# Performance work log

Hardware: AMD Instinct MI355X
Metric: run time of the kernel (lower is better)

Reference implementation:

```python
import jax, jax.numpy as jnp
import numpy as np

EMBED_DIM = 1024
NUM_HEADS = 16
HEAD_DIM = EMBED_DIM // NUM_HEADS
B, S = 2, 2048


def setup_inputs() -> dict:
    key = jax.random.key(0)
    ks = jax.random.split(key, 9)
    d = EMBED_DIM
    scale = 1.0 / np.sqrt(d)
    inp = {
        "x": jax.random.normal(ks[0], (B, S, d), dtype=jnp.float32),
        "mask": jnp.ones((B, S), dtype=jnp.int32),
        "Wq": jax.random.normal(ks[1], (d, d), dtype=jnp.float32) * scale,
        "bq": jnp.zeros((d,), dtype=jnp.float32),
        "Wk": jax.random.normal(ks[2], (d, d), dtype=jnp.float32) * scale,
        "bk": jnp.zeros((d,), dtype=jnp.float32),
        "Wv": jax.random.normal(ks[3], (d, d), dtype=jnp.float32) * scale,
        "bv": jnp.zeros((d,), dtype=jnp.float32),
        "Wo": jax.random.normal(ks[4], (d, d), dtype=jnp.float32) * scale,
        "bo": jnp.zeros((d,), dtype=jnp.float32),
    }
    return inp


def reference(x, mask, Wq, bq, Wk, bk, Wv, bv, Wo, bo):
    b, s, _ = x.shape
    # projections; torch Linear computes x @ W.T + b
    q = (x @ Wq.T + bq).reshape(b, s, NUM_HEADS, HEAD_DIM).transpose(0, 2, 1, 3)
    k = (x @ Wk.T + bk).reshape(b, s, NUM_HEADS, HEAD_DIM).transpose(0, 2, 1, 3)
    v = (x @ Wv.T + bv).reshape(b, s, NUM_HEADS, HEAD_DIM).transpose(0, 2, 1, 3)
    scores = jnp.einsum("bhqd,bhkd->bhqk", q, k) / np.sqrt(HEAD_DIM)  # (B,H,S,S)
    m = (mask == 0)[:, None, None, :]  # broadcast over heads and query pos
    scores = jnp.where(m, jnp.float32(-1e9), scores)
    attn = jax.nn.softmax(scores, axis=-1)
    out = jnp.einsum("bhqk,bhkd->bhqd", attn, v)
    out = out.transpose(0, 2, 1, 3).reshape(b, s, EMBED_DIM)
    return out @ Wo.T + bo
```

## Files before the change

### kernel.cpp

```cpp
#include <hip/hip_runtime.h>

#define EMBED 1024
#define NHEAD 16
#define HDIM  64
#define BB    2
#define SS    2048

typedef __bf16 bf16x8 __attribute__((ext_vector_type(8)));
typedef float  f32x4  __attribute__((ext_vector_type(4)));
typedef _Float16 f16x4 __attribute__((ext_vector_type(4)));
typedef __fp16 hf16x2 __attribute__((ext_vector_type(2)));

__device__ __forceinline__ unsigned short f2bf(float f) {
  union { float f; unsigned u; } v; v.f = f;
  unsigned r = v.u + 0x7fffu + ((v.u >> 16) & 1u);
  return (unsigned short)(r >> 16);
}

__device__ __forceinline__ unsigned short f2h(float f) {
  union { _Float16 h; unsigned short u; } t;
  t.h = (_Float16)f;
  return t.u;
}

__device__ __forceinline__ void g2l16(const unsigned short* g, unsigned short* l) {
  __builtin_amdgcn_global_load_lds(
      (const __attribute__((address_space(1))) unsigned int*)g,
      (__attribute__((address_space(3))) unsigned int*)l, 16, 0, 0);
}

__global__ __launch_bounds__(256)
void cvt5_kernel(const float* __restrict__ x,  const float* __restrict__ Wq,
                 const float* __restrict__ Wk, const float* __restrict__ Wv,
                 const float* __restrict__ Wo,
                 unsigned short* __restrict__ xb,  unsigned short* __restrict__ Wqb,
                 unsigned short* __restrict__ Wkb, unsigned short* __restrict__ Wvb,
                 unsigned short* __restrict__ Wob) {
  const int i = blockIdx.x * 256 + threadIdx.x;
  const float* src;
  unsigned short* dst;
  int j;
  if (i < (1 << 20)) {
    src = x; dst = xb; j = i;
  } else {
    const int t = i - (1 << 20);
    const int r = t >> 18;
    j = t & ((1 << 18) - 1);
    src = (r == 0) ? Wq : (r == 1) ? Wk : (r == 2) ? Wv : Wo;
    dst = (r == 0) ? Wqb : (r == 1) ? Wkb : (r == 2) ? Wvb : Wob;
  }
  const float4 f = ((const float4*)src)[j];
  ushort4 u;
  u.x = f2bf(f.x); u.y = f2bf(f.y); u.z = f2bf(f.z); u.w = f2bf(f.w);
  ((ushort4*)dst)[j] = u;
}

template <typename EpiFn>
__device__ __forceinline__
void gemm_core(const unsigned short* __restrict__ A,
               const unsigned short* __restrict__ Bm,
               int m0, int n0, EpiFn epi) {
  __shared__ unsigned short sA[128 * 64];
  __shared__ unsigned short sB[128 * 64];
  const int tid = threadIdx.x;
  const int l  = tid & 63;
  const int w  = tid >> 6;
  const int lm = l & 15;
  const int qd = l >> 4;
  const int wm = w & 1;
  const int wn = w >> 1;

  f32x4 acc[4][4];
#pragma unroll
  for (int i = 0; i < 4; ++i)
#pragma unroll
    for (int j = 0; j < 4; ++j) acc[i][j] = (f32x4){0.f, 0.f, 0.f, 0.f};

  for (int k0 = 0; k0 < EMBED; k0 += 64) {
#pragma unroll
    for (int i = 0; i < 4; ++i) {
      const int t = i * 256 + tid;
      const int r = t >> 3;
      const int c = (t & 7) ^ (r & 7);
      unsigned short* lp = &sA[(i * 256 + (w << 6)) * 8];
      g2l16(A + (m0 + r) * EMBED + k0 + c * 8, lp);
      unsigned short* lp2 = &sB[(i * 256 + (w << 6)) * 8];
      g2l16(Bm + (n0 + r) * EMBED + k0 + c * 8, lp2);
    }
    __syncthreads();
#pragma unroll
    for (int kk = 0; kk < 2; ++kk) {
      bf16x8 af[4], bfr[4];
#pragma unroll
      for (int mi = 0; mi < 4; ++mi) {
        const int R = wm * 64 + mi * 16 + lm;
        const int ch = R * 8 + (((kk << 2) + qd) ^ (R & 7));
        af[mi] = *(const bf16x8*)&sA[ch * 8];
      }
#pragma unroll
      for (int ni = 0; ni < 4; ++ni) {
        const int R = wn * 64 + ni * 16 + lm;
        const int ch = R * 8 + (((kk << 2) + qd) ^ (R & 7));
        bfr[ni] = *(const bf16x8*)&sB[ch * 8];
      }
#pragma unroll
      for (int mi = 0; mi < 4; ++mi)
#pragma unroll
        for (int ni = 0; ni < 4; ++ni)
          acc[mi][ni] = __builtin_amdgcn_mfma_f32_16x16x32_bf16(
              af[mi], bfr[ni], acc[mi][ni], 0, 0, 0);
    }
    __syncthreads();
  }

#pragma unroll
  for (int mi = 0; mi < 4; ++mi)
#pragma unroll
    for (int ni = 0; ni < 4; ++ni) {
      const int mb = m0 + wm * 64 + mi * 16 + qd * 4;
      const int n  = n0 + wn * 64 + ni * 16 + lm;
      epi(acc[mi][ni], mb, n);
    }
}

__global__ __launch_bounds__(256)
void gemm_qkv(const unsigned short* __restrict__ xb,
              const unsigned short* __restrict__ Wqb,
              const unsigned short* __restrict__ Wkb,
              const unsigned short* __restrict__ Wvb,
              const float* __restrict__ bq, const float* __restrict__ bk,
              const float* __restrict__ bv,
              unsigned short* __restrict__ Qb, unsigned short* __restrict__ Kb,
              unsigned short* __restrict__ VTb) {
  const int z = blockIdx.y;
  const int flat = blockIdx.x;
  if (z < 2) {
    const unsigned short* A = z ? Wkb : Wqb;
    const float* bias = z ? bk : bq;
    unsigned short* O = z ? Kb : Qb;
    const float scale = z ? 1.0f : 0.125f * 1.4426950408889634f;
    const int m0 = (flat >> 5) * 128;
    const int n0 = (flat & 31) * 128;
    gemm_core(A, xb, m0, n0, [&](const f32x4& v, int mb, int n) {
      const float4 bvv = *(const float4*)&bias[mb];
      const int h = mb >> 6, d0 = mb & 63;
      const int b = n >> 11, s = n & 2047;
      ushort4 u;
      u.x = f2bf((v.x + bvv.x) * scale); u.y = f2bf((v.y + bvv.y) * scale);
      u.z = f2bf((v.z + bvv.z) * scale); u.w = f2bf((v.w + bvv.w) * scale);
      *(ushort4*)&O[(((b * NHEAD + h) * SS) + s) * HDIM + d0] = u;
    });
  } else {
    const int m0 = (flat & 31) * 128;
    const int n0 = (flat >> 5) * 128;
    gemm_core(xb, Wvb, m0, n0, [&](const f32x4& v, int mb, int n) {
      const float bvv = bv[n];
      const int b = mb >> 11, s = mb & 2047;
      const int h = n >> 6, d = n & 63;
      ushort4 u;
      u.x = f2h(v.x + bvv); u.y = f2h(v.y + bvv);
      u.z = f2h(v.z + bvv); u.w = f2h(v.w + bvv);
      *(ushort4*)&VTb[(((b * NHEAD + h) * HDIM) + d) * SS + s] = u;
    });
  }
}

__global__ __launch_bounds__(256)
void gemm_out(const unsigned short* __restrict__ Wob,
              const unsigned short* __restrict__ Ob,
              const float* __restrict__ bo, float* __restrict__ out) {
  const int m0 = blockIdx.y * 128;
  const int n0 = blockIdx.x * 128;
  gemm_core(Wob, Ob, m0, n0, [&](const f32x4& v, int mb, int n) {
    const float4 bvv = *(const float4*)&bo[mb];
    float4 o;
    o.x = v.x + bvv.x; o.y = v.y + bvv.y; o.z = v.z + bvv.z; o.w = v.w + bvv.w;
    *(float4*)&out[n * EMBED + mb] = o;
  });
}

__global__ __launch_bounds__(256)
void attn_kernel(const unsigned short* __restrict__ Q,
                 const unsigned short* __restrict__ K,
                 const unsigned short* __restrict__ VT,
                 const int* __restrict__ mask,
                 unsigned short* __restrict__ Obuf) {
  __shared__ unsigned short sK[64 * 64];
  __shared__ unsigned short sV[64 * 64];
  const int tid = threadIdx.x;
  const int l = tid & 63, w = tid >> 6;
  const int lm = l & 15, qd = l >> 4;
  const int b = blockIdx.z, h = blockIdx.y;
  const int q0 = blockIdx.x * 64 + w * 16;
  const unsigned short* Qh = Q + ((b * NHEAD + h) * SS) * HDIM;
  const unsigned short* Kh = K + ((b * NHEAD + h) * SS) * HDIM;
  const unsigned short* Vh = VT + ((b * NHEAD + h) * HDIM) * SS;
  const int* mrow = mask + b * SS;

  const bf16x8 qf0 = *(const bf16x8*)&Qh[(q0 + lm) * HDIM + qd * 8];
  const bf16x8 qf1 = *(const bf16x8*)&Qh[(q0 + lm) * HDIM + 32 + qd * 8];

  f32x4 Od[4];
#pragma unroll
  for (int i = 0; i < 4; ++i) Od[i] = (f32x4){0.f, 0.f, 0.f, 0.f};
  float lsum = 0.f;

  for (int kb = 0; kb < SS; kb += 64) {
#pragma unroll
    for (int i = 0; i < 2; ++i) {
      const int t = i * 256 + tid;
      const int r = t >> 3;
      const int c = (t & 7) ^ (r & 7);
      g2l16(Kh + (kb + r) * HDIM + c * 8, &sK[(i * 256 + (w << 6)) * 8]);
      g2l16(Vh + r * SS + kb + c * 8, &sV[(i * 256 + (w << 6)) * 8]);
    }
    __syncthreads();

    int4 mk[4];
#pragma unroll
    for (int j = 0; j < 4; ++j) mk[j] = *(const int4*)&mrow[kb + j * 16 + qd * 4];

    f32x4 s[4];
#pragma unroll
    for (int j = 0; j < 4; ++j) {
      const int R = j * 16 + lm;
      const bf16x8 k0 = *(const bf16x8*)&sK[(R * 8 + (qd ^ (lm & 7))) * 8];
      const bf16x8 k1 = *(const bf16x8*)&sK[(R * 8 + ((4 + qd) ^ (lm & 7))) * 8];
      f32x4 t0 = (f32x4){0.f, 0.f, 0.f, 0.f};
      t0 = __builtin_amdgcn_mfma_f32_16x16x32_bf16(k0, qf0, t0, 0, 0, 0);
      t0 = __builtin_amdgcn_mfma_f32_16x16x32_bf16(k1, qf1, t0, 0, 0, 0);
      s[j] = t0;
    }

    f16x4 pf[4];
#pragma unroll
    for (int j = 0; j < 4; ++j) {
      const float p0 = mk[j].x ? exp2f(s[j][0]) : 0.f;
      const float p1 = mk[j].y ? exp2f(s[j][1]) : 0.f;
      const float p2 = mk[j].z ? exp2f(s[j][2]) : 0.f;
      const float p3 = mk[j].w ? exp2f(s[j][3]) : 0.f;
      lsum += (p0 + p1) + (p2 + p3);
      union { hf16x2 v[2]; f16x4 f; } pk;
      pk.v[0] = __builtin_amdgcn_cvt_pkrtz(p0, p1);
      pk.v[1] = __builtin_amdgcn_cvt_pkrtz(p2, p3);
      pf[j] = pk.f;
    }

#pragma unroll
    for (int dt = 0; dt < 4; ++dt) {
      const int row = dt * 16 + lm;
#pragma unroll
      for (int j = 0; j < 4; ++j) {
        const int ch = (j * 2 + (qd >> 1)) ^ (lm & 7);
        const f16x4 vf = *(const f16x4*)&sV[row * 64 + ch * 8 + (qd & 1) * 4];
        Od[dt] = __builtin_amdgcn_mfma_f32_16x16x16f16(vf, pf[j], Od[dt], 0, 0, 0);
      }
    }
    __syncthreads();
  }

  lsum += __shfl_xor(lsum, 16);
  lsum += __shfl_xor(lsum, 32);
  const float rinv = 1.f / lsum;
#pragma unroll
  for (int dt = 0; dt < 4; ++dt) {
    ushort4 u;
    u.x = f2bf(Od[dt][0] * rinv); u.y = f2bf(Od[dt][1] * rinv);
    u.z = f2bf(Od[dt][2] * rinv); u.w = f2bf(Od[dt][3] * rinv);
    *(ushort4*)&Obuf[(b * SS + q0 + lm) * EMBED + h * HDIM + dt * 16 + qd * 4] = u;
  }
}

extern "C" void kernel_launch(void* const* d_in, const int* in_sizes, int n_in,
                              void* d_out, int out_size, void* d_ws, size_t ws_size,
                              hipStream_t stream) {
  const float* x  = (const float*)d_in[0];
  const int* mask = (const int*)d_in[1];
  const float* Wq = (const float*)d_in[2];
  const float* bq = (const float*)d_in[3];
  const float* Wk = (const float*)d_in[4];
  const float* bk = (const float*)d_in[5];
  const float* Wv = (const float*)d_in[6];
  const float* bv = (const float*)d_in[7];
  const float* Wo = (const float*)d_in[8];
  const float* bo = (const float*)d_in[9];
  float* out = (float*)d_out;

  char* ws = (char*)d_ws;
  unsigned short* xb  = (unsigned short*)(ws);
  unsigned short* Wqb = (unsigned short*)(ws + 8u * 1024 * 1024);
  unsigned short* Wkb = Wqb + 1024 * 1024;
  unsigned short* Wvb = Wkb + 1024 * 1024;
  unsigned short* Wob = Wvb + 1024 * 1024;
  unsigned short* Qb  = (unsigned short*)(ws + 16u * 1024 * 1024);
  unsigned short* Kb  = Qb + 4u * 1024 * 1024;
  unsigned short* VTb = Kb + 4u * 1024 * 1024;
  unsigned short* Ob  = VTb + 4u * 1024 * 1024;

  cvt5_kernel<<<8192, 256, 0, stream>>>(x, Wq, Wk, Wv, Wo, xb, Wqb, Wkb, Wvb, Wob);
  gemm_qkv<<<dim3(256, 3), 256, 0, stream>>>(xb, Wqb, Wkb, Wvb, bq, bk, bv,
                                             Qb, Kb, VTb);
  attn_kernel<<<dim3(32, 16, 2), 256, 0, stream>>>(Qb, Kb, VTb, mask, Ob);
  gemm_out<<<dim3(32, 8), 256, 0, stream>>>(Wob, Ob, bo, out);
}
```

Measured before the change: 230.9 us.

## Double query rows per attention wave, precompute additive mask bias, swizzle GEMM tiles

Each attention wave now handles 32 query rows instead of 16, so every K/V tile loaded into LDS and every K fragment read feeds twice as many MFMAs. The int mask is turned once, in the conversion kernel, into an additive float bias that seeds the score accumulator, which removes the per-element select. exp2 now uses the hardware builtin. GEMM blocks are remapped in grouped tiles for better L2 reuse. The trade-offs are higher register pressure and only 512 attention blocks, which could lower occupancy.

```diff
diff --git a/kernel.cpp b/kernel.cpp
--- a/kernel.cpp
+++ b/kernel.cpp
@@ -11,6 +11,16 @@
 typedef _Float16 f16x4 __attribute__((ext_vector_type(4)));
 typedef __fp16 hf16x2 __attribute__((ext_vector_type(2)));
 
+#if defined(__has_builtin)
+#if __has_builtin(__builtin_amdgcn_exp2f)
+#define EXP2(x) __builtin_amdgcn_exp2f(x)
+#else
+#define EXP2(x) exp2f(x)
+#endif
+#else
+#define EXP2(x) exp2f(x)
+#endif
+
 __device__ __forceinline__ unsigned short f2bf(float f) {
   union { float f; unsigned u; } v; v.f = f;
   unsigned r = v.u + 0x7fffu + ((v.u >> 16) & 1u);
@@ -32,27 +42,36 @@
 __global__ __launch_bounds__(256)
 void cvt5_kernel(const float* __restrict__ x,  const float* __restrict__ Wq,
                  const float* __restrict__ Wk, const float* __restrict__ Wv,
-                 const float* __restrict__ Wo,
+                 const float* __restrict__ Wo, const int* __restrict__ mask,
                  unsigned short* __restrict__ xb,  unsigned short* __restrict__ Wqb,
                  unsigned short* __restrict__ Wkb, unsigned short* __restrict__ Wvb,
-                 unsigned short* __restrict__ Wob) {
+                 unsigned short* __restrict__ Wob, float* __restrict__ mbias) {
   const int i = blockIdx.x * 256 + threadIdx.x;
-  const float* src;
-  unsigned short* dst;
-  int j;
-  if (i < (1 << 20)) {
-    src = x; dst = xb; j = i;
+  if (i < (1 << 21)) {
+    const float* src;
+    unsigned short* dst;
+    int j;
+    if (i < (1 << 20)) {
+      src = x; dst = xb; j = i;
+    } else {
+      const int t = i - (1 << 20);
+      const int r = t >> 18;
+      j = t & ((1 << 18) - 1);
+      src = (r == 0) ? Wq : (r == 1) ? Wk : (r == 2) ? Wv : Wo;
+      dst = (r == 0) ? Wqb : (r == 1) ? Wkb : (r == 2) ? Wvb : Wob;
+    }
+    const float4 f = ((const float4*)src)[j];
+    ushort4 u;
+    u.x = f2bf(f.x); u.y = f2bf(f.y); u.z = f2bf(f.z); u.w = f2bf(f.w);
+    ((ushort4*)dst)[j] = u;
   } else {
-    const int t = i - (1 << 20);
-    const int r = t >> 18;
-    j = t & ((1 << 18) - 1);
-    src = (r == 0) ? Wq : (r == 1) ? Wk : (r == 2) ? Wv : Wo;
-    dst = (r == 0) ? Wqb : (r == 1) ? Wkb : (r == 2) ? Wvb : Wob;
-  }
-  const float4 f = ((const float4*)src)[j];
-  ushort4 u;
-  u.x = f2bf(f.x); u.y = f2bf(f.y); u.z = f2bf(f.z); u.w = f2bf(f.w);
-  ((ushort4*)dst)[j] = u;
+    const int j = i - (1 << 21);
+    const int4 m = ((const int4*)mask)[j];
+    float4 o;
+    o.x = m.x ? 0.f : -1e30f; o.y = m.y ? 0.f : -1e30f;
+    o.z = m.z ? 0.f : -1e30f; o.w = m.w ? 0.f : -1e30f;
+    ((float4*)mbias)[j] = o;
+  }
 }
 
 template <typename EpiFn>
@@ -82,10 +101,8 @@
       const int t = i * 256 + tid;
       const int r = t >> 3;
       const int c = (t & 7) ^ (r & 7);
-      unsigned short* lp = &sA[(i * 256 + (w << 6)) * 8];
-      g2l16(A + (m0 + r) * EMBED + k0 + c * 8, lp);
-      unsigned short* lp2 = &sB[(i * 256 + (w << 6)) * 8];
-      g2l16(Bm + (n0 + r) * EMBED + k0 + c * 8, lp2);
+      g2l16(A + (m0 + r) * EMBED + k0 + c * 8, &sA[(i * 256 + (w << 6)) * 8]);
+      g2l16(Bm + (n0 + r) * EMBED + k0 + c * 8, &sB[(i * 256 + (w << 6)) * 8]);
     }
     __syncthreads();
 #pragma unroll
@@ -121,6 +138,13 @@
       const int n  = n0 + wn * 64 + ni * 16 + lm;
       epi(acc[mi][ni], mb, n);
     }
+}
+
+__device__ __forceinline__ void decode_tile(int flat, int& a0, int& b0) {
+  const int sub = flat & 15;
+  const int g = flat >> 4;
+  a0 = ((g >> 2) * 2 + (sub >> 3));
+  b0 = ((g & 3) * 8 + (sub & 7));
 }
 
 __global__ __launch_bounds__(256)
@@ -133,15 +157,14 @@
               unsigned short* __restrict__ Qb, unsigned short* __restrict__ Kb,
               unsigned short* __restrict__ VTb) {
   const int z = blockIdx.y;
-  const int flat = blockIdx.x;
+  int a0, b0;
+  decode_tile(blockIdx.x, a0, b0);
   if (z < 2) {
     const unsigned short* A = z ? Wkb : Wqb;
     const float* bias = z ? bk : bq;
     unsigned short* O = z ? Kb : Qb;
     const float scale = z ? 1.0f : 0.125f * 1.4426950408889634f;
-    const int m0 = (flat >> 5) * 128;
-    const int n0 = (flat & 31) * 128;
-    gemm_core(A, xb, m0, n0, [&](const f32x4& v, int mb, int n) {
+    gemm_core(A, xb, a0 * 128, b0 * 128, [&](const f32x4& v, int mb, int n) {
       const float4 bvv = *(const float4*)&bias[mb];
       const int h = mb >> 6, d0 = mb & 63;
       const int b = n >> 11, s = n & 2047;
@@ -151,9 +174,7 @@
       *(ushort4*)&O[(((b * NHEAD + h) * SS) + s) * HDIM + d0] = u;
     });
   } else {
-    const int m0 = (flat & 31) * 128;
-    const int n0 = (flat >> 5) * 128;
-    gemm_core(xb, Wvb, m0, n0, [&](const f32x4& v, int mb, int n) {
+    gemm_core(xb, Wvb, b0 * 128, a0 * 128, [&](const f32x4& v, int mb, int n) {
       const float bvv = bv[n];
       const int b = mb >> 11, s = mb & 2047;
       const int h = n >> 6, d = n & 63;
@@ -169,9 +190,9 @@
 void gemm_out(const unsigned short* __restrict__ Wob,
               const unsigned short* __restrict__ Ob,
               const float* __restrict__ bo, float* __restrict__ out) {
-  const int m0 = blockIdx.y * 128;
-  const int n0 = blockIdx.x * 128;
-  gemm_core(Wob, Ob, m0, n0, [&](const f32x4& v, int mb, int n) {
+  int a0, b0;
+  decode_tile(blockIdx.x, a0, b0);
+  gemm_core(Wob, Ob, a0 * 128, b0 * 128, [&](const f32x4& v, int mb, int n) {
     const float4 bvv = *(const float4*)&bo[mb];
     float4 o;
     o.x = v.x + bvv.x; o.y = v.y + bvv.y; o.z = v.z + bvv.z; o.w = v.w + bvv.w;
@@ -183,7 +204,7 @@
 void attn_kernel(const unsigned short* __restrict__ Q,
                  const unsigned short* __restrict__ K,
                  const unsigned short* __restrict__ VT,
-                 const int* __restrict__ mask,
+                 const float* __restrict__ mbias,
                  unsigned short* __restrict__ Obuf) {
   __shared__ unsigned short sK[64 * 64];
   __shared__ unsigned short sV[64 * 64];
@@ -191,19 +212,25 @@
   const int l = tid & 63, w = tid >> 6;
   const int lm = l & 15, qd = l >> 4;
   const int b = blockIdx.z, h = blockIdx.y;
-  const int q0 = blockIdx.x * 64 + w * 16;
+  const int q0 = blockIdx.x * 128 + w * 32;
   const unsigned short* Qh = Q + ((b * NHEAD + h) * SS) * HDIM;
   const unsigned short* Kh = K + ((b * NHEAD + h) * SS) * HDIM;
   const unsigned short* Vh = VT + ((b * NHEAD + h) * HDIM) * SS;
-  const int* mrow = mask + b * SS;
-
-  const bf16x8 qf0 = *(const bf16x8*)&Qh[(q0 + lm) * HDIM + qd * 8];
-  const bf16x8 qf1 = *(const bf16x8*)&Qh[(q0 + lm) * HDIM + 32 + qd * 8];
-
-  f32x4 Od[4];
-#pragma unroll
-  for (int i = 0; i < 4; ++i) Od[i] = (f32x4){0.f, 0.f, 0.f, 0.f};
-  float lsum = 0.f;
+  const float* mb = mbias + b * SS;
+
+  bf16x8 qf[2][2];
+#pragma unroll
+  for (int g = 0; g < 2; ++g) {
+    qf[g][0] = *(const bf16x8*)&Qh[(q0 + g * 16 + lm) * HDIM + qd * 8];
+    qf[g][1] = *(const bf16x8*)&Qh[(q0 + g * 16 + lm) * HDIM + 32 + qd * 8];
+  }
+
+  f32x4 Od[2][4];
+#pragma unroll
+  for (int g = 0; g < 2; ++g)
+#pragma unroll
+    for (int i = 0; i < 4; ++i) Od[g][i] = (f32x4){0.f, 0.f, 0.f, 0.f};
+  float lsum[2] = {0.f, 0.f};
 
   for (int kb = 0; kb < SS; kb += 64) {
 #pragma unroll
@@ -216,34 +243,29 @@
     }
     __syncthreads();
 
-    int4 mk[4];
-#pragma unroll
-    for (int j = 0; j < 4; ++j) mk[j] = *(const int4*)&mrow[kb + j * 16 + qd * 4];
-
-    f32x4 s[4];
+    f16x4 pf[2][4];
 #pragma unroll
     for (int j = 0; j < 4; ++j) {
       const int R = j * 16 + lm;
       const bf16x8 k0 = *(const bf16x8*)&sK[(R * 8 + (qd ^ (lm & 7))) * 8];
       const bf16x8 k1 = *(const bf16x8*)&sK[(R * 8 + ((4 + qd) ^ (lm & 7))) * 8];
-      f32x4 t0 = (f32x4){0.f, 0.f, 0.f, 0.f};
-      t0 = __builtin_amdgcn_mfma_f32_16x16x32_bf16(k0, qf0, t0, 0, 0, 0);
-      t0 = __builtin_amdgcn_mfma_f32_16x16x32_bf16(k1, qf1, t0, 0, 0, 0);
-      s[j] = t0;
-    }
-
-    f16x4 pf[4];
-#pragma unroll
-    for (int j = 0; j < 4; ++j) {
-      const float p0 = mk[j].x ? exp2f(s[j][0]) : 0.f;
-      const float p1 = mk[j].y ? exp2f(s[j][1]) : 0.f;
-      const float p2 = mk[j].z ? exp2f(s[j][2]) : 0.f;
-      const float p3 = mk[j].w ? exp2f(s[j][3]) : 0.f;
-      lsum += (p0 + p1) + (p2 + p3);
-      union { hf16x2 v[2]; f16x4 f; } pk;
-      pk.v[0] = __builtin_amdgcn_cvt_pkrtz(p0, p1);
-      pk.v[1] = __builtin_amdgcn_cvt_pkrtz(p2, p3);
-      pf[j] = pk.f;
+      const float4 bj = *(const float4*)&mb[kb + j * 16 + qd * 4];
+      const f32x4 binit = (f32x4){bj.x, bj.y, bj.z, bj.w};
+#pragma unroll
+      for (int g = 0; g < 2; ++g) {
+        f32x4 t0 = binit;
+        t0 = __builtin_amdgcn_mfma_f32_16x16x32_bf16(k0, qf[g][0], t0, 0, 0, 0);
+        t0 = __builtin_amdgcn_mfma_f32_16x16x32_bf16(k1, qf[g][1], t0, 0, 0, 0);
+        const float p0 = EXP2(t0[0]);
+        const float p1 = EXP2(t0[1]);
+        const float p2 = EXP2(t0[2]);
+        const float p3 = EXP2(t0[3]);
+        lsum[g] += (p0 + p1) + (p2 + p3);
+        union { hf16x2 v[2]; f16x4 f; } pk;
+        pk.v[0] = __builtin_amdgcn_cvt_pkrtz(p0, p1);
+        pk.v[1] = __builtin_amdgcn_cvt_pkrtz(p2, p3);
+        pf[g][j] = pk.f;
+      }
     }
 
 #pragma unroll
@@ -253,21 +275,29 @@
       for (int j = 0; j < 4; ++j) {
         const int ch = (j * 2 + (qd >> 1)) ^ (lm & 7);
         const f16x4 vf = *(const f16x4*)&sV[row * 64 + ch * 8 + (qd & 1) * 4];
-        Od[dt] = __builtin_amdgcn_mfma_f32_16x16x16f16(vf, pf[j], Od[dt], 0, 0, 0);
+#pragma unroll
+        for (int g = 0; g < 2; ++g)
+          Od[g][dt] = __builtin_amdgcn_mfma_f32_16x16x16f16(vf, pf[g][j],
+                                                            Od[g][dt], 0, 0, 0);
       }
     }
     __syncthreads();
   }
 
-  lsum += __shfl_xor(lsum, 16);
-  lsum += __shfl_xor(lsum, 32);
-  const float rinv = 1.f / lsum;
-#pragma unroll
-  for (int dt = 0; dt < 4; ++dt) {
-    ushort4 u;
-    u.x = f2bf(Od[dt][0] * rinv); u.y = f2bf(Od[dt][1] * rinv);
-    u.z = f2bf(Od[dt][2] * rinv); u.w = f2bf(Od[dt][3] * rinv);
-    *(ushort4*)&Obuf[(b * SS + q0 + lm) * EMBED + h * HDIM + dt * 16 + qd * 4] = u;
+#pragma unroll
+  for (int g = 0; g < 2; ++g) {
+    float ls = lsum[g];
+    ls += __shfl_xor(ls, 16);
+    ls += __shfl_xor(ls, 32);
+    const float rinv = 1.f / ls;
+#pragma unroll
+    for (int dt = 0; dt < 4; ++dt) {
+      ushort4 u;
+      u.x = f2bf(Od[g][dt][0] * rinv); u.y = f2bf(Od[g][dt][1] * rinv);
+      u.z = f2bf(Od[g][dt][2] * rinv); u.w = f2bf(Od[g][dt][3] * rinv);
+      *(ushort4*)&Obuf[(b * SS + q0 + g * 16 + lm) * EMBED + h * HDIM +
+                       dt * 16 + qd * 4] = u;
+    }
   }
 }
 
@@ -296,10 +326,12 @@
   unsigned short* Kb  = Qb + 4u * 1024 * 1024;
   unsigned short* VTb = Kb + 4u * 1024 * 1024;
   unsigned short* Ob  = VTb + 4u * 1024 * 1024;
-
-  cvt5_kernel<<<8192, 256, 0, stream>>>(x, Wq, Wk, Wv, Wo, xb, Wqb, Wkb, Wvb, Wob);
+  float* mbb = (float*)(ws + 48u * 1024 * 1024);
+
+  cvt5_kernel<<<8196, 256, 0, stream>>>(x, Wq, Wk, Wv, Wo, mask,
+                                        xb, Wqb, Wkb, Wvb, Wob, mbb);
   gemm_qkv<<<dim3(256, 3), 256, 0, stream>>>(xb, Wqb, Wkb, Wvb, bq, bk, bv,
                                              Qb, Kb, VTb);
-  attn_kernel<<<dim3(32, 16, 2), 256, 0, stream>>>(Qb, Kb, VTb, mask, Ob);
-  gemm_out<<<dim3(32, 8), 256, 0, stream>>>(Wob, Ob, bo, out);
-}
+  attn_kernel<<<dim3(16, 16, 2), 256, 0, stream>>>(Qb, Kb, VTb, mbb, Ob);
+  gemm_out<<<256, 256, 0, stream>>>(Wob, Ob, bo, out);
+}
```

After: 219.8 us. 1.05x faster.
